# Optimization experiments

Measured on AMD Instinct MI355X. Metric: run time of the kernel, lower is better.

## Reference

```python
import jax, jax.numpy as jnp
import numpy as np
from jax.scipy.special import logsumexp

B, T, H, S = 32, 2000, 256, 63  # batch, time steps, hidden dim, num_states (=num_classes)


def setup_inputs() -> dict:
    key = jax.random.key(0)
    ks = jax.random.split(key, 5)
    return {
        "ctc_logits": jax.random.normal(ks[0], (B, T, S), dtype=jnp.float32),
        "frame_embeddings": jax.random.normal(ks[1], (B, T, H), dtype=jnp.float32),
        "keyword_tokens": jax.random.randint(ks[2], (B, 32), 0, S),
        "W1": jax.random.normal(ks[3], (2 * H, H), dtype=jnp.float32) * 0.02,
        "b1": jnp.zeros((H,), dtype=jnp.float32),
        "W2": jax.random.normal(ks[4], (H, S), dtype=jnp.float32) * 0.02,
        "b2": jnp.zeros((S,), dtype=jnp.float32),
    }


def reference(ctc_logits, frame_embeddings, keyword_tokens, W1, b1, W2, b2):
    Bv, Tv, Sv = ctc_logits.shape
    logp = jax.nn.log_softmax(ctc_logits, axis=-1)  # (B,T,S)

    # transition scores for frame pair (t, t-1) <-> trans_all[t-1], batched over all t at once
    pairs = jnp.concatenate([frame_embeddings[:, 1:], frame_embeddings[:, :-1]], axis=-1)  # (B,T-1,2H)
    h = jax.nn.relu(jnp.einsum("bti,ij->btj", pairs, W1) + b1)
    trans = jnp.einsum("bti,ij->btj", h, W2) + b2  # (B,T-1,S)

    lp_t = jnp.swapaxes(logp, 0, 1)   # (T,B,S)
    tr_t = jnp.swapaxes(trans, 0, 1)  # (T-1,B,S)

    # forward recursion
    f0 = jnp.zeros((Bv, Sv), dtype=logp.dtype).at[:, 0].set(
        logp[jnp.arange(Bv), 0, keyword_tokens[:, 0]])

    def fstep(f_prev, x):
        lp, tr = x  # each (B,S)
        # [b,j,s] = f_prev[b,j] + lp[b,s] + tr[b,s]; reduce over j (prev state)
        scores = f_prev[:, :, None] + lp[:, None, :] + tr[:, None, :]
        f = logsumexp(scores, axis=1)
        return f, f

    _, f_rest = jax.lax.scan(fstep, f0, (lp_t[1:], tr_t))
    fwd = jnp.concatenate([f0[None], f_rest], axis=0)  # (T,B,S)

    # backward recursion (reverse scan); backward at t uses pair (t+1, t) = trans[t]
    bT = jnp.zeros((Bv, Sv), dtype=logp.dtype)

    def bstep(b_next, x):
        lp, tr = x  # lp = logp[t+1], tr = trans[t]
        # [b,s,k] = b_next[b,k] + lp[b,s] + tr[b,s]; reduce over k (next state)
        scores = b_next[:, None, :] + lp[:, :, None] + tr[:, :, None]
        b = logsumexp(scores, axis=2)
        return b, b

    _, b_rest = jax.lax.scan(bstep, bT, (lp_t[1:], tr_t), reverse=True)
    bwd = jnp.concatenate([b_rest, bT[None]], axis=0)  # (T,B,S)

    alignments = jax.nn.softmax(jnp.swapaxes(fwd + bwd, 0, 1), axis=-1)  # (B,T,S)
    return alignments
```

## Files before the change

### kernel.cpp

```cpp
#include <hip/hip_runtime.h>
#include <stdint.h>

#define NB 32
#define NT 2000
#define NH 256
#define NS 63
#define LDSROW 264

typedef __attribute__((ext_vector_type(8))) short bf16x8;
typedef __attribute__((ext_vector_type(4))) float f32x4;

__device__ inline unsigned short f2bf(float f) {
  union { float f; uint32_t u; } v; v.f = f;
  return (unsigned short)((v.u + 0x7fffu + ((v.u >> 16) & 1u)) >> 16);
}
__device__ inline unsigned int pk2(float a, float b) {
  return (unsigned int)f2bf(a) | ((unsigned int)f2bf(b) << 16);
}
__device__ inline bf16x8 pack8(const float* g) {
  union { bf16x8 v; unsigned int u[4]; } c;
  c.u[0] = pk2(g[0], g[1]); c.u[1] = pk2(g[2], g[3]);
  c.u[2] = pk2(g[4], g[5]); c.u[3] = pk2(g[6], g[7]);
  return c.v;
}

__device__ inline unsigned int pk2_hw(float a, float b) {
  unsigned int r;
  asm("v_cvt_pk_bf16_f32 %0, %1, %2" : "=v"(r) : "v"(a), "v"(b));
  return r;
}
__device__ inline unsigned short cvt1_hw(float a) {
  unsigned int r;
  asm("v_cvt_pk_bf16_f32 %0, %1, %1" : "=v"(r) : "v"(a));
  return (unsigned short)r;
}

#define NSLOT1 (16 * 4 * 4 * 64)
#define NSLOT2 (8 * 4 * 64)
#define WS_NEEDED ((size_t)(NSLOT1 + NSLOT2) * 16)

__global__ __launch_bounds__(256) void prep_weights(
    const float* __restrict__ W1, const float* __restrict__ W2,
    unsigned short* __restrict__ w1f, unsigned short* __restrict__ w2f) {
  const int tid = blockIdx.x * 256 + threadIdx.x;
  if (tid < NSLOT1) {
    const int lane = tid & 63;
    const int quad = lane >> 4, l16 = lane & 15;
    int r = tid >> 6;
    const int tn = r & 3; r >>= 2;
    const int wv = r & 3; r >>= 2;
    const int km = r;
    const int kb = (km >> 3) * 256 + (km & 7) * 32 + quad * 8;
    const int n = wv * 64 + tn * 16 + l16;
    ushort4 lo, hi;
    lo.x = f2bf(W1[(size_t)(kb + 0) * NH + n]);
    lo.y = f2bf(W1[(size_t)(kb + 1) * NH + n]);
    lo.z = f2bf(W1[(size_t)(kb + 2) * NH + n]);
    lo.w = f2bf(W1[(size_t)(kb + 3) * NH + n]);
    hi.x = f2bf(W1[(size_t)(kb + 4) * NH + n]);
    hi.y = f2bf(W1[(size_t)(kb + 5) * NH + n]);
    hi.z = f2bf(W1[(size_t)(kb + 6) * NH + n]);
    hi.w = f2bf(W1[(size_t)(kb + 7) * NH + n]);
    *(ushort4*)&w1f[(size_t)tid * 8] = lo;
    *(ushort4*)&w1f[(size_t)tid * 8 + 4] = hi;
  } else if (tid < NSLOT1 + NSLOT2) {
    const int t2 = tid - NSLOT1;
    const int lane = t2 & 63;
    const int quad = lane >> 4, l16 = lane & 15;
    const int tn = (t2 >> 6) & 3;
    const int ks = t2 >> 8;
    const int kb = ks * 32 + quad * 8;
    const int n = tn * 16 + l16;
    ushort4 lo = {0, 0, 0, 0}, hi = {0, 0, 0, 0};
    if (n < NS) {
      lo.x = f2bf(W2[(size_t)(kb + 0) * NS + n]);
      lo.y = f2bf(W2[(size_t)(kb + 1) * NS + n]);
      lo.z = f2bf(W2[(size_t)(kb + 2) * NS + n]);
      lo.w = f2bf(W2[(size_t)(kb + 3) * NS + n]);
      hi.x = f2bf(W2[(size_t)(kb + 4) * NS + n]);
      hi.y = f2bf(W2[(size_t)(kb + 5) * NS + n]);
      hi.z = f2bf(W2[(size_t)(kb + 6) * NS + n]);
      hi.w = f2bf(W2[(size_t)(kb + 7) * NS + n]);
    }
    *(ushort4*)&w2f[(size_t)t2 * 8] = lo;
    *(ushort4*)&w2f[(size_t)t2 * 8 + 4] = hi;
  }
}

template <bool PACKED>
__global__ __launch_bounds__(256, 4) void fused_kernel(
    const float* __restrict__ E, const float* __restrict__ logits,
    const int* __restrict__ kw,
    const float* __restrict__ W1, const float* __restrict__ W2,
    const unsigned short* __restrict__ w1f, const unsigned short* __restrict__ w2f,
    const float* __restrict__ b1, const float* __restrict__ b2,
    float* __restrict__ out) {
  const int b = blockIdx.y;
  const int a0 = blockIdx.x * 63;
  const int base = a0 - 1;
  const int tid = threadIdx.x;
  const int w = tid >> 6;
  const int lane = tid & 63;
  const int quad = lane >> 4;
  const int l16 = lane & 15;
  const int n0 = w * 64;

  __shared__ unsigned short lds[65 * LDSROW];
  float* TRf = (float*)lds;

  const float* Eb = E + (size_t)b * NT * NH;
  const float* lb = logits + (size_t)b * NT * NS;

  #pragma unroll
  for (int it = 0; it < 16; ++it) {
    const int row = it * 4 + w;
    int tr = base + row;
    tr = (tr < 0) ? 0 : (tr > NT - 1 ? NT - 1 : tr);
    float4 v = *(const float4*)&Eb[(size_t)tr * NH + (lane << 2)];
    uint2 o;
    o.x = pk2_hw(v.x, v.y); o.y = pk2_hw(v.z, v.w);
    *(uint2*)&lds[row * LDSROW + (lane << 2)] = o;
  }
  if (tid < 64) {
    int tr = base + 64; if (tr > NT - 1) tr = NT - 1;
    float4 v = *(const float4*)&Eb[(size_t)tr * NH + (lane << 2)];
    uint2 o;
    o.x = pk2_hw(v.x, v.y); o.y = pk2_hw(v.z, v.w);
    *(uint2*)&lds[64 * LDSROW + (lane << 2)] = o;
  }
  __syncthreads();

  f32x4 acc[4][4];
  #pragma unroll
  for (int tm = 0; tm < 4; ++tm)
    #pragma unroll
    for (int tn = 0; tn < 4; ++tn) acc[tm][tn] = (f32x4){0.f, 0.f, 0.f, 0.f};

  if constexpr (PACKED) {
    const unsigned short* wbase = w1f + (size_t)(((w << 2) * 64) + lane) * 8;
#define W1F_AT(KM, TN) \
  (*(const bf16x8*)(wbase + ((size_t)((((KM) << 4) + (TN))) << 9)))
    bf16x8 cb0 = W1F_AT(0, 0), cb1 = W1F_AT(0, 1);
    bf16x8 cb2 = W1F_AT(0, 2), cb3 = W1F_AT(0, 3);
    __builtin_amdgcn_s_setprio(1);
    #pragma unroll
    for (int km = 0; km < 16; ++km) {
      bf16x8 nb0, nb1, nb2, nb3;
      if (km < 15) {
        nb0 = W1F_AT(km + 1, 0); nb1 = W1F_AT(km + 1, 1);
        nb2 = W1F_AT(km + 1, 2); nb3 = W1F_AT(km + 1, 3);
      }
      const int aoff = (km >> 3) ? 0 : 1;
      bf16x8 af[4];
      #pragma unroll
      for (int tm = 0; tm < 4; ++tm)
        af[tm] = *(const bf16x8*)&lds[(tm * 16 + l16 + aoff) * LDSROW +
                                      (km & 7) * 32 + quad * 8];
      #pragma unroll
      for (int tm = 0; tm < 4; ++tm)
        acc[tm][0] = __builtin_amdgcn_mfma_f32_16x16x32_bf16(af[tm], cb0, acc[tm][0], 0, 0, 0);
      #pragma unroll
      for (int tm = 0; tm < 4; ++tm)
        acc[tm][1] = __builtin_amdgcn_mfma_f32_16x16x32_bf16(af[tm], cb1, acc[tm][1], 0, 0, 0);
      #pragma unroll
      for (int tm = 0; tm < 4; ++tm)
        acc[tm][2] = __builtin_amdgcn_mfma_f32_16x16x32_bf16(af[tm], cb2, acc[tm][2], 0, 0, 0);
      #pragma unroll
      for (int tm = 0; tm < 4; ++tm)
        acc[tm][3] = __builtin_amdgcn_mfma_f32_16x16x32_bf16(af[tm], cb3, acc[tm][3], 0, 0, 0);
      if (km < 15) { cb0 = nb0; cb1 = nb1; cb2 = nb2; cb3 = nb3; }
    }
    __builtin_amdgcn_s_setprio(0);
#undef W1F_AT
  } else {
    const float* w1p = W1 + (size_t)(quad * 8) * NH + n0 + l16;
    #pragma unroll
    for (int km = 0; km < 16; ++km) {
      const int hk = (km >> 3) * 256 + (km & 7) * 32;
      const int aoff = (km >> 3) ? 0 : 1;
      bf16x8 af[4];
      #pragma unroll
      for (int tm = 0; tm < 4; ++tm)
        af[tm] = *(const bf16x8*)&lds[(tm * 16 + l16 + aoff) * LDSROW +
                                      (km & 7) * 32 + quad * 8];
      float g[8], gn[8];
      #pragma unroll
      for (int j = 0; j < 8; ++j) g[j] = w1p[(size_t)(hk + j) * NH];
      #pragma unroll
      for (int tn = 0; tn < 4; ++tn) {
        if (tn < 3) {
          #pragma unroll
          for (int j = 0; j < 8; ++j)
            gn[j] = w1p[(size_t)(hk + j) * NH + (tn + 1) * 16];
        }
        bf16x8 bq = pack8(g);
        #pragma unroll
        for (int tm = 0; tm < 4; ++tm)
          acc[tm][tn] = __builtin_amdgcn_mfma_f32_16x16x32_bf16(
              af[tm], bq, acc[tm][tn], 0, 0, 0);
        if (tn < 3) {
          #pragma unroll
          for (int j = 0; j < 8; ++j) g[j] = gn[j];
        }
      }
    }
  }
  __syncthreads();

  #pragma unroll
  for (int tn = 0; tn < 4; ++tn) {
    float b1v = b1[n0 + tn * 16 + l16];
    #pragma unroll
    for (int tm = 0; tm < 4; ++tm)
      #pragma unroll
      for (int r = 0; r < 4; ++r) {
        float hv = fmaxf(acc[tm][tn][r] + b1v, 0.f);
        lds[(tm * 16 + quad * 4 + r) * LDSROW + n0 + tn * 16 + l16] = cvt1_hw(hv);
      }
  }
  __syncthreads();

  const int m0 = w * 16;
  float lpv[16];
  #pragma unroll
  for (int tn = 0; tn < 4; ++tn) {
    const int s = tn * 16 + l16;
    const int cc = (s < NS) ? s : NS - 1;
    #pragma unroll
    for (int r = 0; r < 4; ++r) {
      int tt = a0 + m0 + quad * 4 + r;
      if (tt > NT - 1) tt = NT - 1;
      lpv[tn * 4 + r] = lb[(size_t)tt * NS + cc];
    }
  }

  f32x4 acc2[4];
  #pragma unroll
  for (int tn = 0; tn < 4; ++tn) acc2[tn] = (f32x4){0.f, 0.f, 0.f, 0.f};

  if constexpr (PACKED) {
    const unsigned short* w2base = w2f + (size_t)lane * 8;
    __builtin_amdgcn_s_setprio(1);
    #pragma unroll
    for (int ks = 0; ks < 8; ++ks) {
      bf16x8 af = *(const bf16x8*)&lds[(m0 + l16) * LDSROW + ks * 32 + quad * 8];
      #pragma unroll
      for (int tn = 0; tn < 4; ++tn) {
        bf16x8 bq = *(const bf16x8*)(w2base + ((size_t)((ks << 2) + tn) << 9));
        acc2[tn] = __builtin_amdgcn_mfma_f32_16x16x32_bf16(af, bq, acc2[tn], 0, 0, 0);
      }
    }
    __builtin_amdgcn_s_setprio(0);
  } else {
    #pragma unroll
    for (int ks = 0; ks < 8; ++ks) {
      const int k0 = ks * 32;
      bf16x8 af = *(const bf16x8*)&lds[(m0 + l16) * LDSROW + k0 + quad * 8];
      #pragma unroll
      for (int tn = 0; tn < 4; ++tn) {
        const int n = tn * 16 + l16;
        float g[8];
        #pragma unroll
        for (int j = 0; j < 8; ++j)
          g[j] = (n < NS) ? W2[(size_t)(k0 + quad * 8 + j) * NS + n] : 0.f;
        bf16x8 bq = pack8(g);
        acc2[tn] = __builtin_amdgcn_mfma_f32_16x16x32_bf16(af, bq, acc2[tn], 0, 0, 0);
      }
    }
  }
  __syncthreads();

  #pragma unroll
  for (int tn = 0; tn < 4; ++tn) {
    const int s = tn * 16 + l16;
    const float b2v = (s < NS) ? b2[s] : 0.f;
    #pragma unroll
    for (int r = 0; r < 4; ++r)
      TRf[(m0 + quad * 4 + r) * 68 + s] = acc2[tn][r] + b2v + lpv[tn * 4 + r];
  }
  __syncthreads();

  if (a0 == 0 && w == 0) {
    float v = (lane < NS) ? lb[lane] : -1e30f;
    float m = v;
    #pragma unroll
    for (int o = 32; o > 0; o >>= 1) m = fmaxf(m, __shfl_xor(m, o));
    float ee = (lane < NS) ? __expf(v - m) : 0.f;
    float ss = ee;
    #pragma unroll
    for (int o = 32; o > 0; o >>= 1) ss += __shfl_xor(ss, o);
    const float lse = m + __logf(ss);
    const float f00 = lb[kw[b * 32]] - lse;
    float sc = ((lane == 0) ? f00 : 0.f) + TRf[68 + lane];
    float e = (lane < NS) ? __expf(sc) : 0.f;
    float s = e;
    #pragma unroll
    for (int o = 32; o > 0; o >>= 1) s += __shfl_xor(s, o);
    if (lane < NS)
      out[(size_t)b * NT * NS + lane] = e * __builtin_amdgcn_rcpf(s);
  }

  float ev[16], sm[16];
  #pragma unroll
  for (int rr = 0; rr < 16; ++rr) {
    const int j = m0 + rr;
    const int t = a0 + j;
    const bool valid = (j < 63) && (t < NT) && (t != 0);
    float u0 = valid ? TRf[j * 68 + lane] : 0.f;
    float u1 = (valid && t != NT - 1) ? TRf[(j + 1) * 68 + lane] : 0.f;
    ev[rr] = (valid && lane < NS) ? __expf(u0 + u1) : 0.f;
    sm[rr] = ev[rr];
  }
  #pragma unroll
  for (int o = 32; o > 0; o >>= 1) {
    #pragma unroll
    for (int rr = 0; rr < 16; ++rr) sm[rr] += __shfl_xor(sm[rr], o);
  }
  #pragma unroll
  for (int rr = 0; rr < 16; ++rr) {
    const int j = m0 + rr;
    const int t = a0 + j;
    const bool valid = (j < 63) && (t < NT) && (t != 0);
    if (valid && lane < NS)
      out[((size_t)b * NT + t) * NS + lane] = ev[rr] * __builtin_amdgcn_rcpf(sm[rr]);
  }
}

extern "C" void kernel_launch(void* const* d_in, const int* in_sizes, int n_in,
                              void* d_out, int out_size, void* d_ws, size_t ws_size,
                              hipStream_t stream) {
  const float* logits = (const float*)d_in[0];
  const float* E      = (const float*)d_in[1];
  const int*   kw     = (const int*)d_in[2];
  const float* W1     = (const float*)d_in[3];
  const float* b1     = (const float*)d_in[4];
  const float* W2     = (const float*)d_in[5];
  const float* b2     = (const float*)d_in[6];
  float* out = (float*)d_out;

  dim3 g(32, NB);

  if (ws_size >= WS_NEEDED && d_ws != nullptr) {
    unsigned short* w1f = (unsigned short*)d_ws;
    unsigned short* w2f = w1f + (size_t)NSLOT1 * 8;
    prep_weights<<<dim3((NSLOT1 + NSLOT2) / 256), 256, 0, stream>>>(W1, W2, w1f, w2f);
    fused_kernel<true><<<g, 256, 0, stream>>>(E, logits, kw, W1, W2, w1f, w2f,
                                              b1, b2, out);
  } else {
    fused_kernel<false><<<g, 256, 0, stream>>>(E, logits, kw, W1, W2, nullptr,
                                               nullptr, b1, b2, out);
  }
}
```

Before: 134.1 us.

## Process two time tiles per block and prefetch the next tile during GEMM2

Each block now has 512 threads and handles two consecutive 63-step tiles, so the grid is halved. Two LDS buffers are used: while waves 0-3 run the second GEMM and write transition scores for the current tile, waves 4-7 load and convert the next tile's frame embeddings into the other buffer. The first GEMM is split across 8 waves with 32 output columns each. The aim is to hide global-load latency for the second tile and reuse block setup, at the cost of doubling LDS per block, which may reduce the number of resident blocks, and idling half the waves during the second GEMM.

```diff
diff --git a/kernel.cpp b/kernel.cpp
--- a/kernel.cpp
+++ b/kernel.cpp
@@ -6,6 +6,7 @@
 #define NH 256
 #define NS 63
 #define LDSROW 264
+#define TILE_USH (65 * LDSROW)
 
 typedef __attribute__((ext_vector_type(8))) short bf16x8;
 typedef __attribute__((ext_vector_type(4))) float f32x4;
@@ -23,7 +24,6 @@
   c.u[2] = pk2(g[4], g[5]); c.u[3] = pk2(g[6], g[7]);
   return c.v;
 }
-
 __device__ inline unsigned int pk2_hw(float a, float b) {
   unsigned int r;
   asm("v_cvt_pk_bf16_f32 %0, %1, %2" : "=v"(r) : "v"(a), "v"(b));
@@ -88,7 +88,225 @@
 }
 
 template <bool PACKED>
-__global__ __launch_bounds__(256, 4) void fused_kernel(
+__device__ __forceinline__ void process_tile(
+    unsigned short* Rc, unsigned short* Rn, int a0, int baseNext, bool stageNext,
+    const float* __restrict__ Eb, const float* __restrict__ lb,
+    const int* __restrict__ kw,
+    const float* __restrict__ W1, const float* __restrict__ W2,
+    const unsigned short* __restrict__ w1f, const unsigned short* __restrict__ w2f,
+    const float* __restrict__ b1, const float* __restrict__ b2,
+    float* __restrict__ out, int b, int w, int lane, int quad, int l16) {
+  const int n0c = w * 32;
+
+  f32x4 acc[4][2];
+  #pragma unroll
+  for (int tm = 0; tm < 4; ++tm) {
+    acc[tm][0] = (f32x4){0.f, 0.f, 0.f, 0.f};
+    acc[tm][1] = (f32x4){0.f, 0.f, 0.f, 0.f};
+  }
+
+  if constexpr (PACKED) {
+    const unsigned short* wb = w1f + (size_t)lane * 8 + ((size_t)(w << 1) << 9);
+#define W1F_AT(KM, TT) \
+  (*(const bf16x8*)(wb + ((size_t)((((KM) << 4) + (TT))) << 9)))
+    bf16x8 c0 = W1F_AT(0, 0), c1 = W1F_AT(0, 1);
+    __builtin_amdgcn_s_setprio(1);
+    #pragma unroll
+    for (int km = 0; km < 16; ++km) {
+      bf16x8 p0, p1;
+      if (km < 15) { p0 = W1F_AT(km + 1, 0); p1 = W1F_AT(km + 1, 1); }
+      const int aoff = (km >> 3) ? 0 : 1;
+      bf16x8 af[4];
+      #pragma unroll
+      for (int tm = 0; tm < 4; ++tm)
+        af[tm] = *(const bf16x8*)&Rc[(tm * 16 + l16 + aoff) * LDSROW +
+                                     (km & 7) * 32 + quad * 8];
+      #pragma unroll
+      for (int tm = 0; tm < 4; ++tm)
+        acc[tm][0] = __builtin_amdgcn_mfma_f32_16x16x32_bf16(af[tm], c0, acc[tm][0], 0, 0, 0);
+      #pragma unroll
+      for (int tm = 0; tm < 4; ++tm)
+        acc[tm][1] = __builtin_amdgcn_mfma_f32_16x16x32_bf16(af[tm], c1, acc[tm][1], 0, 0, 0);
+      if (km < 15) { c0 = p0; c1 = p1; }
+    }
+    __builtin_amdgcn_s_setprio(0);
+#undef W1F_AT
+  } else {
+    const float* w1p = W1 + (size_t)(quad * 8) * NH + n0c + l16;
+    #pragma unroll
+    for (int km = 0; km < 16; ++km) {
+      const int hk = (km >> 3) * 256 + (km & 7) * 32;
+      const int aoff = (km >> 3) ? 0 : 1;
+      bf16x8 af[4];
+      #pragma unroll
+      for (int tm = 0; tm < 4; ++tm)
+        af[tm] = *(const bf16x8*)&Rc[(tm * 16 + l16 + aoff) * LDSROW +
+                                     (km & 7) * 32 + quad * 8];
+      #pragma unroll
+      for (int tt = 0; tt < 2; ++tt) {
+        float g[8];
+        #pragma unroll
+        for (int j = 0; j < 8; ++j)
+          g[j] = w1p[(size_t)(hk + j) * NH + tt * 16];
+        bf16x8 bq = pack8(g);
+        #pragma unroll
+        for (int tm = 0; tm < 4; ++tm)
+          acc[tm][tt] = __builtin_amdgcn_mfma_f32_16x16x32_bf16(
+              af[tm], bq, acc[tm][tt], 0, 0, 0);
+      }
+    }
+  }
+  __syncthreads();
+
+  #pragma unroll
+  for (int tt = 0; tt < 2; ++tt) {
+    float b1v = b1[n0c + tt * 16 + l16];
+    #pragma unroll
+    for (int tm = 0; tm < 4; ++tm)
+      #pragma unroll
+      for (int r = 0; r < 4; ++r) {
+        float hv = fmaxf(acc[tm][tt][r] + b1v, 0.f);
+        Rc[(tm * 16 + quad * 4 + r) * LDSROW + n0c + tt * 16 + l16] = cvt1_hw(hv);
+      }
+  }
+  __syncthreads();
+
+  if (w < 4) {
+    const int m0 = w * 16;
+    float lpv[16];
+    #pragma unroll
+    for (int tn = 0; tn < 4; ++tn) {
+      const int s = tn * 16 + l16;
+      const int cc = (s < NS) ? s : NS - 1;
+      #pragma unroll
+      for (int r = 0; r < 4; ++r) {
+        int tt2 = a0 + m0 + quad * 4 + r;
+        if (tt2 > NT - 1) tt2 = NT - 1;
+        lpv[tn * 4 + r] = lb[(size_t)tt2 * NS + cc];
+      }
+    }
+    f32x4 acc2[4];
+    #pragma unroll
+    for (int tn = 0; tn < 4; ++tn) acc2[tn] = (f32x4){0.f, 0.f, 0.f, 0.f};
+
+    if constexpr (PACKED) {
+      const unsigned short* w2base = w2f + (size_t)lane * 8;
+      __builtin_amdgcn_s_setprio(1);
+      #pragma unroll
+      for (int ks = 0; ks < 8; ++ks) {
+        bf16x8 af = *(const bf16x8*)&Rc[(m0 + l16) * LDSROW + ks * 32 + quad * 8];
+        #pragma unroll
+        for (int tn = 0; tn < 4; ++tn) {
+          bf16x8 bq = *(const bf16x8*)(w2base + ((size_t)((ks << 2) + tn) << 9));
+          acc2[tn] = __builtin_amdgcn_mfma_f32_16x16x32_bf16(af, bq, acc2[tn], 0, 0, 0);
+        }
+      }
+      __builtin_amdgcn_s_setprio(0);
+    } else {
+      #pragma unroll
+      for (int ks = 0; ks < 8; ++ks) {
+        const int k0 = ks * 32;
+        bf16x8 af = *(const bf16x8*)&Rc[(m0 + l16) * LDSROW + k0 + quad * 8];
+        #pragma unroll
+        for (int tn = 0; tn < 4; ++tn) {
+          const int n = tn * 16 + l16;
+          float g[8];
+          #pragma unroll
+          for (int j = 0; j < 8; ++j)
+            g[j] = (n < NS) ? W2[(size_t)(k0 + quad * 8 + j) * NS + n] : 0.f;
+          bf16x8 bq = pack8(g);
+          acc2[tn] = __builtin_amdgcn_mfma_f32_16x16x32_bf16(af, bq, acc2[tn], 0, 0, 0);
+        }
+      }
+    }
+    float* Uw = (float*)(Rc + (size_t)m0 * LDSROW);
+    #pragma unroll
+    for (int tn = 0; tn < 4; ++tn) {
+      const int s = tn * 16 + l16;
+      const float b2v = (s < NS) ? b2[s] : 0.f;
+      #pragma unroll
+      for (int r = 0; r < 4; ++r)
+        Uw[(quad * 4 + r) * 68 + s] = acc2[tn][r] + b2v + lpv[tn * 4 + r];
+    }
+  } else if (stageNext) {
+    const int wd = w - 4;
+    float4 eb[16];
+    #pragma unroll
+    for (int it = 0; it < 16; ++it) {
+      int tr = baseNext + it * 4 + wd;
+      tr = (tr < 0) ? 0 : (tr > NT - 1 ? NT - 1 : tr);
+      eb[it] = *(const float4*)&Eb[(size_t)tr * NH + (lane << 2)];
+    }
+    float4 e64;
+    if (wd == 0) {
+      int tr = baseNext + 64; if (tr > NT - 1) tr = NT - 1;
+      e64 = *(const float4*)&Eb[(size_t)tr * NH + (lane << 2)];
+    }
+    #pragma unroll
+    for (int it = 0; it < 16; ++it) {
+      const int row = it * 4 + wd;
+      uint2 o; o.x = pk2_hw(eb[it].x, eb[it].y); o.y = pk2_hw(eb[it].z, eb[it].w);
+      *(uint2*)&Rn[row * LDSROW + (lane << 2)] = o;
+    }
+    if (wd == 0) {
+      uint2 o; o.x = pk2_hw(e64.x, e64.y); o.y = pk2_hw(e64.z, e64.w);
+      *(uint2*)&Rn[64 * LDSROW + (lane << 2)] = o;
+    }
+  }
+  __syncthreads();
+
+  if (a0 == 0 && w == 0) {
+    float v = (lane < NS) ? lb[lane] : -1e30f;
+    float m = v;
+    #pragma unroll
+    for (int o = 32; o > 0; o >>= 1) m = fmaxf(m, __shfl_xor(m, o));
+    float ee = (lane < NS) ? __expf(v - m) : 0.f;
+    float ss = ee;
+    #pragma unroll
+    for (int o = 32; o > 0; o >>= 1) ss += __shfl_xor(ss, o);
+    const float lse = m + __logf(ss);
+    const float f00 = lb[kw[b * 32]] - lse;
+    const float* Ur = (const float*)Rc;
+    float sc = ((lane == 0) ? f00 : 0.f) + Ur[68 + lane];
+    float e = (lane < NS) ? __expf(sc) : 0.f;
+    float s = e;
+    #pragma unroll
+    for (int o = 32; o > 0; o >>= 1) s += __shfl_xor(s, o);
+    if (lane < NS)
+      out[(size_t)b * NT * NS + lane] = e * __builtin_amdgcn_rcpf(s);
+  }
+
+  const float* Ur = (const float*)Rc;
+  float ev[8], sm[8];
+  #pragma unroll
+  for (int rr = 0; rr < 8; ++rr) {
+    const int j = w * 8 + rr;
+    const int t = a0 + j;
+    const bool valid = (j < 63) && (t < NT) && (t != 0);
+    float u0 = valid ? Ur[(j >> 4) * 2112 + (j & 15) * 68 + lane] : 0.f;
+    float u1 = (valid && t != NT - 1)
+                   ? Ur[((j + 1) >> 4) * 2112 + ((j + 1) & 15) * 68 + lane]
+                   : 0.f;
+    ev[rr] = (valid && lane < NS) ? __expf(u0 + u1) : 0.f;
+    sm[rr] = ev[rr];
+  }
+  #pragma unroll
+  for (int o = 32; o > 0; o >>= 1) {
+    #pragma unroll
+    for (int rr = 0; rr < 8; ++rr) sm[rr] += __shfl_xor(sm[rr], o);
+  }
+  #pragma unroll
+  for (int rr = 0; rr < 8; ++rr) {
+    const int j = w * 8 + rr;
+    const int t = a0 + j;
+    const bool valid = (j < 63) && (t < NT) && (t != 0);
+    if (valid && lane < NS)
+      out[((size_t)b * NT + t) * NS + lane] = ev[rr] * __builtin_amdgcn_rcpf(sm[rr]);
+  }
+}
+
+template <bool PACKED>
+__global__ __launch_bounds__(512, 4) void fused_kernel(
     const float* __restrict__ E, const float* __restrict__ logits,
     const int* __restrict__ kw,
     const float* __restrict__ W1, const float* __restrict__ W2,
@@ -96,234 +314,46 @@
     const float* __restrict__ b1, const float* __restrict__ b2,
     float* __restrict__ out) {
   const int b = blockIdx.y;
-  const int a0 = blockIdx.x * 63;
-  const int base = a0 - 1;
+  const int bx = blockIdx.x;
+  const int a0A = bx * 126;
+  const int a0B = a0A + 63;
   const int tid = threadIdx.x;
   const int w = tid >> 6;
   const int lane = tid & 63;
   const int quad = lane >> 4;
   const int l16 = lane & 15;
-  const int n0 = w * 64;
-
-  __shared__ unsigned short lds[65 * LDSROW];
-  float* TRf = (float*)lds;
+
+  extern __shared__ unsigned short lds[];
+  unsigned short* RA = lds;
+  unsigned short* RB = lds + TILE_USH;
 
   const float* Eb = E + (size_t)b * NT * NH;
   const float* lb = logits + (size_t)b * NT * NS;
 
-  #pragma unroll
-  for (int it = 0; it < 16; ++it) {
-    const int row = it * 4 + w;
-    int tr = base + row;
-    tr = (tr < 0) ? 0 : (tr > NT - 1 ? NT - 1 : tr);
-    float4 v = *(const float4*)&Eb[(size_t)tr * NH + (lane << 2)];
-    uint2 o;
-    o.x = pk2_hw(v.x, v.y); o.y = pk2_hw(v.z, v.w);
-    *(uint2*)&lds[row * LDSROW + (lane << 2)] = o;
-  }
-  if (tid < 64) {
-    int tr = base + 64; if (tr > NT - 1) tr = NT - 1;
-    float4 v = *(const float4*)&Eb[(size_t)tr * NH + (lane << 2)];
-    uint2 o;
-    o.x = pk2_hw(v.x, v.y); o.y = pk2_hw(v.z, v.w);
-    *(uint2*)&lds[64 * LDSROW + (lane << 2)] = o;
+  {
+    const int base = a0A - 1;
+    #pragma unroll
+    for (int it = 0; it < 8; ++it) {
+      const int row = it * 8 + w;
+      int tr = base + row;
+      tr = (tr < 0) ? 0 : (tr > NT - 1 ? NT - 1 : tr);
+      float4 v = *(const float4*)&Eb[(size_t)tr * NH + (lane << 2)];
+      uint2 o; o.x = pk2_hw(v.x, v.y); o.y = pk2_hw(v.z, v.w);
+      *(uint2*)&RA[row * LDSROW + (lane << 2)] = o;
+    }
+    if (w == 0) {
+      int tr = base + 64; if (tr > NT - 1) tr = NT - 1;
+      float4 v = *(const float4*)&Eb[(size_t)tr * NH + (lane << 2)];
+      uint2 o; o.x = pk2_hw(v.x, v.y); o.y = pk2_hw(v.z, v.w);
+      *(uint2*)&RA[64 * LDSROW + (lane << 2)] = o;
+    }
   }
   __syncthreads();
 
-  f32x4 acc[4][4];
-  #pragma unroll
-  for (int tm = 0; tm < 4; ++tm)
-    #pragma unroll
-    for (int tn = 0; tn < 4; ++tn) acc[tm][tn] = (f32x4){0.f, 0.f, 0.f, 0.f};
-
-  if constexpr (PACKED) {
-    const unsigned short* wbase = w1f + (size_t)(((w << 2) * 64) + lane) * 8;
-#define W1F_AT(KM, TN) \
-  (*(const bf16x8*)(wbase + ((size_t)((((KM) << 4) + (TN))) << 9)))
-    bf16x8 cb0 = W1F_AT(0, 0), cb1 = W1F_AT(0, 1);
-    bf16x8 cb2 = W1F_AT(0, 2), cb3 = W1F_AT(0, 3);
-    __builtin_amdgcn_s_setprio(1);
-    #pragma unroll
-    for (int km = 0; km < 16; ++km) {
-      bf16x8 nb0, nb1, nb2, nb3;
-      if (km < 15) {
-        nb0 = W1F_AT(km + 1, 0); nb1 = W1F_AT(km + 1, 1);
-        nb2 = W1F_AT(km + 1, 2); nb3 = W1F_AT(km + 1, 3);
-      }
-      const int aoff = (km >> 3) ? 0 : 1;
-      bf16x8 af[4];
-      #pragma unroll
-      for (int tm = 0; tm < 4; ++tm)
-        af[tm] = *(const bf16x8*)&lds[(tm * 16 + l16 + aoff) * LDSROW +
-                                      (km & 7) * 32 + quad * 8];
-      #pragma unroll
-      for (int tm = 0; tm < 4; ++tm)
-        acc[tm][0] = __builtin_amdgcn_mfma_f32_16x16x32_bf16(af[tm], cb0, acc[tm][0], 0, 0, 0);
-      #pragma unroll
-      for (int tm = 0; tm < 4; ++tm)
-        acc[tm][1] = __builtin_amdgcn_mfma_f32_16x16x32_bf16(af[tm], cb1, acc[tm][1], 0, 0, 0);
-      #pragma unroll
-      for (int tm = 0; tm < 4; ++tm)
-        acc[tm][2] = __builtin_amdgcn_mfma_f32_16x16x32_bf16(af[tm], cb2, acc[tm][2], 0, 0, 0);
-      #pragma unroll
-      for (int tm = 0; tm < 4; ++tm)
-        acc[tm][3] = __builtin_amdgcn_mfma_f32_16x16x32_bf16(af[tm], cb3, acc[tm][3], 0, 0, 0);
-      if (km < 15) { cb0 = nb0; cb1 = nb1; cb2 = nb2; cb3 = nb3; }
-    }
-    __builtin_amdgcn_s_setprio(0);
-#undef W1F_AT
-  } else {
-    const float* w1p = W1 + (size_t)(quad * 8) * NH + n0 + l16;
-    #pragma unroll
-    for (int km = 0; km < 16; ++km) {
-      const int hk = (km >> 3) * 256 + (km & 7) * 32;
-      const int aoff = (km >> 3) ? 0 : 1;
-      bf16x8 af[4];
-      #pragma unroll
-      for (int tm = 0; tm < 4; ++tm)
-        af[tm] = *(const bf16x8*)&lds[(tm * 16 + l16 + aoff) * LDSROW +
-                                      (km & 7) * 32 + quad * 8];
-      float g[8], gn[8];
-      #pragma unroll
-      for (int j = 0; j < 8; ++j) g[j] = w1p[(size_t)(hk + j) * NH];
-      #pragma unroll
-      for (int tn = 0; tn < 4; ++tn) {
-        if (tn < 3) {
-          #pragma unroll
-          for (int j = 0; j < 8; ++j)
-            gn[j] = w1p[(size_t)(hk + j) * NH + (tn + 1) * 16];
-        }
-        bf16x8 bq = pack8(g);
-        #pragma unroll
-        for (int tm = 0; tm < 4; ++tm)
-          acc[tm][tn] = __builtin_amdgcn_mfma_f32_16x16x32_bf16(
-              af[tm], bq, acc[tm][tn], 0, 0, 0);
-        if (tn < 3) {
-          #pragma unroll
-          for (int j = 0; j < 8; ++j) g[j] = gn[j];
-        }
-      }
-    }
-  }
-  __syncthreads();
-
-  #pragma unroll
-  for (int tn = 0; tn < 4; ++tn) {
-    float b1v = b1[n0 + tn * 16 + l16];
-    #pragma unroll
-    for (int tm = 0; tm < 4; ++tm)
-      #pragma unroll
-      for (int r = 0; r < 4; ++r) {
-        float hv = fmaxf(acc[tm][tn][r] + b1v, 0.f);
-        lds[(tm * 16 + quad * 4 + r) * LDSROW + n0 + tn * 16 + l16] = cvt1_hw(hv);
-      }
-  }
-  __syncthreads();
-
-  const int m0 = w * 16;
-  float lpv[16];
-  #pragma unroll
-  for (int tn = 0; tn < 4; ++tn) {
-    const int s = tn * 16 + l16;
-    const int cc = (s < NS) ? s : NS - 1;
-    #pragma unroll
-    for (int r = 0; r < 4; ++r) {
-      int tt = a0 + m0 + quad * 4 + r;
-      if (tt > NT - 1) tt = NT - 1;
-      lpv[tn * 4 + r] = lb[(size_t)tt * NS + cc];
-    }
-  }
-
-  f32x4 acc2[4];
-  #pragma unroll
-  for (int tn = 0; tn < 4; ++tn) acc2[tn] = (f32x4){0.f, 0.f, 0.f, 0.f};
-
-  if constexpr (PACKED) {
-    const unsigned short* w2base = w2f + (size_t)lane * 8;
-    __builtin_amdgcn_s_setprio(1);
-    #pragma unroll
-    for (int ks = 0; ks < 8; ++ks) {
-      bf16x8 af = *(const bf16x8*)&lds[(m0 + l16) * LDSROW + ks * 32 + quad * 8];
-      #pragma unroll
-      for (int tn = 0; tn < 4; ++tn) {
-        bf16x8 bq = *(const bf16x8*)(w2base + ((size_t)((ks << 2) + tn) << 9));
-        acc2[tn] = __builtin_amdgcn_mfma_f32_16x16x32_bf16(af, bq, acc2[tn], 0, 0, 0);
-      }
-    }
-    __builtin_amdgcn_s_setprio(0);
-  } else {
-    #pragma unroll
-    for (int ks = 0; ks < 8; ++ks) {
-      const int k0 = ks * 32;
-      bf16x8 af = *(const bf16x8*)&lds[(m0 + l16) * LDSROW + k0 + quad * 8];
-      #pragma unroll
-      for (int tn = 0; tn < 4; ++tn) {
-        const int n = tn * 16 + l16;
-        float g[8];
-        #pragma unroll
-        for (int j = 0; j < 8; ++j)
-          g[j] = (n < NS) ? W2[(size_t)(k0 + quad * 8 + j) * NS + n] : 0.f;
-        bf16x8 bq = pack8(g);
-        acc2[tn] = __builtin_amdgcn_mfma_f32_16x16x32_bf16(af, bq, acc2[tn], 0, 0, 0);
-      }
-    }
-  }
-  __syncthreads();
-
-  #pragma unroll
-  for (int tn = 0; tn < 4; ++tn) {
-    const int s = tn * 16 + l16;
-    const float b2v = (s < NS) ? b2[s] : 0.f;
-    #pragma unroll
-    for (int r = 0; r < 4; ++r)
-      TRf[(m0 + quad * 4 + r) * 68 + s] = acc2[tn][r] + b2v + lpv[tn * 4 + r];
-  }
-  __syncthreads();
-
-  if (a0 == 0 && w == 0) {
-    float v = (lane < NS) ? lb[lane] : -1e30f;
-    float m = v;
-    #pragma unroll
-    for (int o = 32; o > 0; o >>= 1) m = fmaxf(m, __shfl_xor(m, o));
-    float ee = (lane < NS) ? __expf(v - m) : 0.f;
-    float ss = ee;
-    #pragma unroll
-    for (int o = 32; o > 0; o >>= 1) ss += __shfl_xor(ss, o);
-    const float lse = m + __logf(ss);
-    const float f00 = lb[kw[b * 32]] - lse;
-    float sc = ((lane == 0) ? f00 : 0.f) + TRf[68 + lane];
-    float e = (lane < NS) ? __expf(sc) : 0.f;
-    float s = e;
-    #pragma unroll
-    for (int o = 32; o > 0; o >>= 1) s += __shfl_xor(s, o);
-    if (lane < NS)
-      out[(size_t)b * NT * NS + lane] = e * __builtin_amdgcn_rcpf(s);
-  }
-
-  float ev[16], sm[16];
-  #pragma unroll
-  for (int rr = 0; rr < 16; ++rr) {
-    const int j = m0 + rr;
-    const int t = a0 + j;
-    const bool valid = (j < 63) && (t < NT) && (t != 0);
-    float u0 = valid ? TRf[j * 68 + lane] : 0.f;
-    float u1 = (valid && t != NT - 1) ? TRf[(j + 1) * 68 + lane] : 0.f;
-    ev[rr] = (valid && lane < NS) ? __expf(u0 + u1) : 0.f;
-    sm[rr] = ev[rr];
-  }
-  #pragma unroll
-  for (int o = 32; o > 0; o >>= 1) {
-    #pragma unroll
-    for (int rr = 0; rr < 16; ++rr) sm[rr] += __shfl_xor(sm[rr], o);
-  }
-  #pragma unroll
-  for (int rr = 0; rr < 16; ++rr) {
-    const int j = m0 + rr;
-    const int t = a0 + j;
-    const bool valid = (j < 63) && (t < NT) && (t != 0);
-    if (valid && lane < NS)
-      out[((size_t)b * NT + t) * NS + lane] = ev[rr] * __builtin_amdgcn_rcpf(sm[rr]);
-  }
+  process_tile<PACKED>(RA, RB, a0A, a0B - 1, true, Eb, lb, kw, W1, W2,
+                       w1f, w2f, b1, b2, out, b, w, lane, quad, l16);
+  process_tile<PACKED>(RB, RA, a0B, 0, false, Eb, lb, kw, W1, W2,
+                       w1f, w2f, b1, b2, out, b, w, lane, quad, l16);
 }
 
 extern "C" void kernel_launch(void* const* d_in, const int* in_sizes, int n_in,
@@ -338,16 +368,17 @@
   const float* b2     = (const float*)d_in[6];
   float* out = (float*)d_out;
 
-  dim3 g(32, NB);
+  dim3 g(16, NB);
+  const size_t shmem = (size_t)2 * TILE_USH * sizeof(unsigned short);
 
   if (ws_size >= WS_NEEDED && d_ws != nullptr) {
     unsigned short* w1f = (unsigned short*)d_ws;
     unsigned short* w2f = w1f + (size_t)NSLOT1 * 8;
     prep_weights<<<dim3((NSLOT1 + NSLOT2) / 256), 256, 0, stream>>>(W1, W2, w1f, w2f);
-    fused_kernel<true><<<g, 256, 0, stream>>>(E, logits, kw, W1, W2, w1f, w2f,
-                                              b1, b2, out);
+    fused_kernel<true><<<g, 512, shmem, stream>>>(E, logits, kw, W1, W2, w1f, w2f,
+                                                  b1, b2, out);
   } else {
-    fused_kernel<false><<<g, 256, 0, stream>>>(E, logits, kw, W1, W2, nullptr,
-                                               nullptr, b1, b2, out);
-  }
-}
+    fused_kernel<false><<<g, 512, shmem, stream>>>(E, logits, kw, W1, W2, nullptr,
+                                                   nullptr, b1, b2, out);
+  }
+}
```

Measured after the change: 160.9 us. 20.0% more time.
